# Performance work log

Measured on AMD Instinct MI355X. Metric: run time of the kernel, lower is better.

The kernel has to match this reference:

```python
import jax, jax.numpy as jnp
import numpy as np

B, T, C, H = 4, 2048, 768, 12
D = C // H  # head dim = 64


def setup_inputs() -> dict:
    key = jax.random.key(0)
    ks = jax.random.split(key, 6)
    scale = 1.0 / np.sqrt(C)
    x = jax.random.normal(ks[0], (B, T, C), dtype=jnp.float32)
    # True = padded key (original passes ~key_padding_mask to SDPA)
    key_padding_mask = jax.random.randint(ks[1], (B, 1, 1, T), 0, 2) == 1
    Wqkv = jax.random.normal(ks[2], (C, 3 * C), dtype=jnp.float32) * scale
    bqkv = jax.random.normal(ks[3], (3 * C,), dtype=jnp.float32) * 0.02
    Wproj = jax.random.normal(ks[4], (C, C), dtype=jnp.float32) * scale
    bproj = jax.random.normal(ks[5], (C,), dtype=jnp.float32) * 0.02
    return {"x": x, "key_padding_mask": key_padding_mask, "Wqkv": Wqkv,
            "bqkv": bqkv, "Wproj": Wproj, "bproj": bproj}


def reference(x, key_padding_mask, Wqkv, bqkv, Wproj, bproj):
    # fused QKV projection
    qkv = x @ Wqkv + bqkv                      # [B,T,3C]
    q, k, v = jnp.split(qkv, 3, axis=-1)       # each [B,T,C]

    def heads(t):  # [B,T,C] -> [B,H,T,D]
        return t.reshape(B, T, H, D).transpose(0, 2, 1, 3)

    q, k, v = heads(q), heads(k), heads(v)
    scores = jnp.einsum('bhqd,bhkd->bhqk', q, k) / np.sqrt(D).astype(jnp.float32)
    # attn_mask = ~key_padding_mask: True means attend; padded keys -> -inf
    scores = jnp.where(key_padding_mask, jnp.finfo(scores.dtype).min, scores)
    attn = jax.nn.softmax(scores, axis=-1)
    y = jnp.einsum('bhqk,bhkd->bhqd', attn, v)  # [B,H,T,D]
    y = y.transpose(0, 2, 1, 3).reshape(B, T, C)
    y = y @ Wproj + bproj
    return y
```

## Files before the change

### kernel.cpp

```cpp
#include <hip/hip_runtime.h>
#include <stdint.h>

#define B_ 4
#define T_ 2048
#define C_ 768
#define H_ 12
#define D_ 64
#define BT_ (B_*T_)
#define C3_ (3*C_)
#define FMIN_ (-3.402823466e38f)
#define QSCALE_ (0.18033688f)

typedef __attribute__((ext_vector_type(8))) short short8;
typedef __attribute__((ext_vector_type(4))) short s16x4;
typedef __attribute__((ext_vector_type(4))) float f32x4;

__device__ __forceinline__ float bf2f(unsigned short u) {
    union { unsigned int i; float f; } v; v.i = ((unsigned int)u) << 16; return v.f;
}
__device__ __forceinline__ unsigned short f2bf(float f) {
    union { float ff; unsigned int i; } v; v.ff = f;
    unsigned int r = v.i + 0x7fffu + ((v.i >> 16) & 1u);
    return (unsigned short)(r >> 16);
}
__device__ __forceinline__ unsigned int cvtpk(float lo, float hi) {
    unsigned int r;
    asm("v_cvt_pk_bf16_f32 %0, %1, %2" : "=v"(r) : "v"(lo), "v"(hi));
    return r;
}
__device__ __forceinline__ float ldf(const void* p, size_t i, int isbf) {
    return isbf ? bf2f(((const unsigned short*)p)[i]) : ((const float*)p)[i];
}

__global__ void k_detect(const void* x, const void* wqkv, const void* bqkv,
                         const void* wproj, const void* bproj, const void* mask,
                         int* flags) {
    __shared__ int cnt[8];
    int tid = threadIdx.x;
    if (tid < 8) cnt[tid] = 0;
    __syncthreads();
    const void* ptrs[5] = {x, wqkv, bqkv, wproj, bproj};
#pragma unroll
    for (int t = 0; t < 5; ++t) {
        unsigned short u = ((const unsigned short*)ptrs[t])[2 * tid];
        int e = (u >> 7) & 0xff;
        if (e >= 100 && e <= 140) atomicAdd(&cnt[t], 1);
    }
    if (tid < 64) {
        unsigned int d = ((const unsigned int*)mask)[tid];
        if (d <= 1u) atomicAdd(&cnt[5], 1);
        if (d == 0u || d == 0x3f800000u) atomicAdd(&cnt[6], 1);
    }
    __syncthreads();
    if (tid < 5) flags[tid] = (cnt[tid] >= 128) ? 1 : 0;
    if (tid == 5) flags[5] = (cnt[5] == 64) ? 1 : ((cnt[6] == 64) ? 2 : 0);
}

__global__ void k_canon_x(const void* x, unsigned short* xb, const int* flags) {
    const int n8 = BT_ * C_ / 8;
    int i = blockIdx.x * blockDim.x + threadIdx.x;
    if (i >= n8) return;
    if (flags[0]) {
        ((int4*)xb)[i] = ((const int4*)x)[i];
    } else {
        const float4* xf = (const float4*)x;
        float4 a = xf[2*i], b = xf[2*i+1];
        short8 o;
        o[0]=(short)f2bf(a.x); o[1]=(short)f2bf(a.y); o[2]=(short)f2bf(a.z); o[3]=(short)f2bf(a.w);
        o[4]=(short)f2bf(b.x); o[5]=(short)f2bf(b.y); o[6]=(short)f2bf(b.z); o[7]=(short)f2bf(b.w);
        *(short8*)&xb[8*i] = o;
    }
}

__global__ void k_canon_wT(const void* src, unsigned short* dst, const int* flags,
                           int fidx, int K, int N) {
    __shared__ float tile[32][33];
    int mode = flags[fidx];
    int n0 = blockIdx.x * 32, k0 = blockIdx.y * 32;
    int tx = threadIdx.x & 31, ty = threadIdx.x >> 5;
    for (int r = ty; r < 32; r += 8) {
        size_t idx = (size_t)(k0 + r) * N + (n0 + tx);
        tile[r][tx] = mode ? bf2f(((const unsigned short*)src)[idx])
                           : ((const float*)src)[idx];
    }
    __syncthreads();
    for (int r = ty; r < 32; r += 8) {
        dst[(size_t)(n0 + r) * K + k0 + tx] = f2bf(tile[tx][r]);
    }
}

__global__ void k_canon_small(const void* bqkv, const void* bproj, const void* mask,
                              float* bqkvF, float* bprojF, float* maskF, const int* flags) {
    int i = blockIdx.x * blockDim.x + threadIdx.x;
    if (i < C3_) bqkvF[i] = ldf(bqkv, i, flags[2]);
    if (i < C_)  bprojF[i] = ldf(bproj, i, flags[4]);
    if (i < BT_) {
        int mm = flags[5];
        int mv;
        if (mm == 1)      mv = ((const int*)mask)[i] != 0;
        else if (mm == 2) mv = ((const float*)mask)[i] != 0.0f;
        else              mv = ((const unsigned char*)mask)[i] != 0;
        maskF[i] = mv ? FMIN_ : 0.0f;
    }
}

template<int EPI>
__global__ __launch_bounds__(256) void k_gemm(
        const unsigned short* __restrict__ A, const unsigned short* __restrict__ Bt,
        const float* __restrict__ bias,
        void* __restrict__ out0, unsigned short* __restrict__ out1,
        unsigned short* __restrict__ out2,
        int M, int N, int K) {
    __shared__ __align__(16) unsigned short la[128*72];
    __shared__ __align__(16) unsigned short lb[128*72];
    const int tid = threadIdx.x;
    const int w = tid >> 6, lane = tid & 63, lr = lane & 15, lg = lane >> 4;
    const int wm = (w >> 1) * 64, wn = (w & 1) * 64;
    const int n0 = blockIdx.x * 128, m0 = blockIdx.y * 128;
    f32x4 acc[4][4] = {};
    for (int k0 = 0; k0 < K; k0 += 64) {
#pragma unroll
        for (int c = 0; c < 4; ++c) {
            int idx = tid + c * 256;
            int row = idx >> 3, c8 = (idx & 7) * 8;
            *(short8*)&la[row*72 + c8] = *(const short8*)&A[(size_t)(m0+row)*K + k0 + c8];
            *(short8*)&lb[row*72 + c8] = *(const short8*)&Bt[(size_t)(n0+row)*K + k0 + c8];
        }
        __syncthreads();
#pragma unroll
        for (int ks = 0; ks < 64; ks += 32) {
            short8 af[4], bfr[4];
#pragma unroll
            for (int i = 0; i < 4; ++i)
                af[i] = *(const short8*)&la[(wm + i*16 + lr)*72 + ks + lg*8];
#pragma unroll
            for (int j = 0; j < 4; ++j)
                bfr[j] = *(const short8*)&lb[(wn + j*16 + lr)*72 + ks + lg*8];
#pragma unroll
            for (int i = 0; i < 4; ++i)
#pragma unroll
                for (int j = 0; j < 4; ++j)
                    acc[i][j] = __builtin_amdgcn_mfma_f32_16x16x32_bf16(af[i], bfr[j], acc[i][j], 0, 0, 0);
        }
        __syncthreads();
    }
#pragma unroll
    for (int i = 0; i < 4; ++i)
#pragma unroll
        for (int j = 0; j < 4; ++j)
#pragma unroll
            for (int r = 0; r < 4; ++r) {
                int row = m0 + wm + i*16 + lg*4 + r;
                int col = n0 + wn + j*16 + lr;
                float v = acc[i][j][r] + bias[col];
                if (EPI == 0) {
                    int seg = col / C_;
                    int c = col - seg * C_;
                    int h = c >> 6, d = c & 63;
                    int b = row >> 11, t = row & (T_ - 1);
                    if (seg == 0)      ((unsigned short*)out0)[(((size_t)b*H_ + h)*T_ + t)*D_ + d] = f2bf(v * QSCALE_);
                    else if (seg == 1) out1[(((size_t)b*H_ + h)*T_ + t)*D_ + d] = f2bf(v);
                    else               out2[(((size_t)b*H_ + h)*D_ + d)*T_ + t] = f2bf(v);
                } else {
                    ((float*)out0)[(size_t)row * N + col] = v;
                }
            }
}

__global__ __launch_bounds__(256) void k_attn(
        const unsigned short* __restrict__ Q, const unsigned short* __restrict__ Kt,
        const unsigned short* __restrict__ Vt, const float* __restrict__ maskF,
        unsigned short* __restrict__ AO) {
    __shared__ __align__(16) unsigned short lk[64*72];
    __shared__ __align__(16) unsigned short lv[64*72];
    __shared__ __align__(16) float lmb[64];
    const int tid = threadIdx.x;
    const int w = tid >> 6, lane = tid & 63, lr = lane & 15, lg = lane >> 4;
    const int per = gridDim.x >> 3;
    const int swz = (blockIdx.x & 7) * per + (blockIdx.x >> 3);
    const int bh = swz >> 4, qt = swz & 15;
    const int b = bh / H_, h = bh - b * H_;
    const int qbase = qt * 128 + w * 32;
    const unsigned short* Qb = Q  + (size_t)bh * T_ * D_;
    const unsigned short* Kb = Kt + (size_t)bh * T_ * D_;
    const unsigned short* Vb = Vt + (size_t)bh * D_ * T_;

    short8 qf[2][2];
#pragma unroll
    for (int qc = 0; qc < 2; ++qc)
#pragma unroll
        for (int dh = 0; dh < 2; ++dh)
            qf[qc][dh] = *(const short8*)&Qb[(size_t)(qbase + qc*16 + lr) * D_ + dh*32 + lg*8];

    f32x4 ot[4][2] = {};
    float m[2] = {-INFINITY, -INFINITY}, l[2] = {0.0f, 0.0f};

    for (int kt = 0; kt < T_; kt += 64) {
#pragma unroll
        for (int c = 0; c < 2; ++c) {
            int idx = tid + c * 256;
            int row = idx >> 3, c8 = (idx & 7) * 8;
            *(short8*)&lk[row*72 + c8] = *(const short8*)&Kb[(size_t)(kt + row)*D_ + c8];
            *(short8*)&lv[row*72 + c8] = *(const short8*)&Vb[(size_t)row * T_ + kt + c8];
        }
        if (tid < 64) lmb[tid] = maskF[b*T_ + kt + tid];
        __syncthreads();

        f32x4 st[4][2];
#pragma unroll
        for (int kf = 0; kf < 4; ++kf) {
            f32x4 mi = *(const f32x4*)&lmb[kf*16 + lg*4];
            st[kf][0] = mi;
            st[kf][1] = mi;
        }
#pragma unroll
        for (int dh = 0; dh < 2; ++dh) {
            short8 kfr[4];
#pragma unroll
            for (int kf = 0; kf < 4; ++kf)
                kfr[kf] = *(const short8*)&lk[(kf*16 + lr)*72 + dh*32 + lg*8];
#pragma unroll
            for (int kf = 0; kf < 4; ++kf)
#pragma unroll
                for (int qc = 0; qc < 2; ++qc)
                    st[kf][qc] = __builtin_amdgcn_mfma_f32_16x16x32_bf16(kfr[kf], qf[qc][dh], st[kf][qc], 0, 0, 0);
        }
#pragma unroll
        for (int qc = 0; qc < 2; ++qc) {
            float t0 = fmaxf(fmaxf(st[0][qc][0], st[0][qc][1]), st[0][qc][2]);
            float t1 = fmaxf(fmaxf(st[0][qc][3], st[1][qc][0]), st[1][qc][1]);
            float t2 = fmaxf(fmaxf(st[1][qc][2], st[1][qc][3]), st[2][qc][0]);
            float t3 = fmaxf(fmaxf(st[2][qc][1], st[2][qc][2]), st[2][qc][3]);
            float t4 = fmaxf(fmaxf(st[3][qc][0], st[3][qc][1]), st[3][qc][2]);
            float tm = fmaxf(fmaxf(t0, t1), fmaxf(fmaxf(t2, t3), fmaxf(t4, st[3][qc][3])));
            tm = fmaxf(tm, __shfl_xor(tm, 16));
            tm = fmaxf(tm, __shfl_xor(tm, 32));
            if (!__all(tm - m[qc] <= 8.0f)) {
                float mn = fmaxf(m[qc], tm);
                float sc = __builtin_amdgcn_exp2f(m[qc] - mn);
                m[qc] = mn;
                l[qc] *= sc;
#pragma unroll
                for (int dblk = 0; dblk < 4; ++dblk) ot[dblk][qc] *= sc;
            }
            float mr = m[qc];
            float ps = 0.0f;
#pragma unroll
            for (int kf = 0; kf < 4; ++kf)
#pragma unroll
                for (int r = 0; r < 4; ++r) {
                    float p = __builtin_amdgcn_exp2f(st[kf][qc][r] - mr);
                    st[kf][qc][r] = p;
                    ps += p;
                }
            l[qc] += ps;
        }
        union PU { unsigned int u[4]; short8 s; };
        PU pb[2][2];
#pragma unroll
        for (int qc = 0; qc < 2; ++qc)
#pragma unroll
            for (int ks = 0; ks < 2; ++ks) {
                pb[qc][ks].u[0] = cvtpk(st[2*ks][qc][0],   st[2*ks][qc][1]);
                pb[qc][ks].u[1] = cvtpk(st[2*ks][qc][2],   st[2*ks][qc][3]);
                pb[qc][ks].u[2] = cvtpk(st[2*ks+1][qc][0], st[2*ks+1][qc][1]);
                pb[qc][ks].u[3] = cvtpk(st[2*ks+1][qc][2], st[2*ks+1][qc][3]);
            }
#pragma unroll
        for (int ks = 0; ks < 2; ++ks)
#pragma unroll
            for (int dblk = 0; dblk < 4; ++dblk) {
                const int rb = (dblk*16 + lr)*72 + 32*ks + lg*4;
                s16x4 lo = *(const s16x4*)&lv[rb];
                s16x4 hi = *(const s16x4*)&lv[rb + 16];
                short8 va;
                va[0]=lo[0]; va[1]=lo[1]; va[2]=lo[2]; va[3]=lo[3];
                va[4]=hi[0]; va[5]=hi[1]; va[6]=hi[2]; va[7]=hi[3];
#pragma unroll
                for (int qc = 0; qc < 2; ++qc)
                    ot[dblk][qc] = __builtin_amdgcn_mfma_f32_16x16x32_bf16(va, pb[qc][ks].s, ot[dblk][qc], 0, 0, 0);
            }
        __syncthreads();
    }
#pragma unroll
    for (int qc = 0; qc < 2; ++qc) {
        float ls = l[qc];
        ls += __shfl_xor(ls, 16);
        ls += __shfl_xor(ls, 32);
        float inv = 1.0f / ls;
        size_t row = (size_t)b*T_ + qbase + qc*16 + lr;
#pragma unroll
        for (int dblk = 0; dblk < 4; ++dblk) {
            unsigned int w0 = cvtpk(ot[dblk][qc][0]*inv, ot[dblk][qc][1]*inv);
            unsigned int w1 = cvtpk(ot[dblk][qc][2]*inv, ot[dblk][qc][3]*inv);
            uint2 pkd; pkd.x = w0; pkd.y = w1;
            *(uint2*)&AO[row * C_ + h*64 + dblk*16 + lg*4] = pkd;
        }
    }
}

extern "C" void kernel_launch(void* const* d_in, const int* in_sizes, int n_in,
                              void* d_out, int out_size, void* d_ws, size_t ws_size,
                              hipStream_t stream) {
    const void* x     = d_in[0];
    const void* mask  = d_in[1];
    const void* wqkv  = d_in[2];
    const void* bqkv  = d_in[3];
    const void* wproj = d_in[4];
    const void* bproj = d_in[5];

    char* ws = (char*)d_ws;
    size_t off = 0;
    auto alloc = [&](size_t bytes) -> void* {
        void* p = ws + off;
        off = (off + bytes + 255) & ~(size_t)255;
        return p;
    };
    int* flags            = (int*)alloc(256);
    unsigned short* Xb    = (unsigned short*)alloc((size_t)BT_ * C_ * 2);
    unsigned short* WqkvT = (unsigned short*)alloc((size_t)C3_ * C_ * 2);
    unsigned short* WprojT= (unsigned short*)alloc((size_t)C_ * C_ * 2);
    float* bqkvF          = (float*)alloc((size_t)C3_ * 4);
    float* bprojF         = (float*)alloc((size_t)C_ * 4);
    float* maskF          = (float*)alloc((size_t)BT_ * 4);
    unsigned short* Qs    = (unsigned short*)alloc((size_t)B_*H_*T_*D_ * 2);
    unsigned short* Ks    = (unsigned short*)alloc((size_t)B_*H_*T_*D_ * 2);
    unsigned short* Vts   = (unsigned short*)alloc((size_t)B_*H_*T_*D_ * 2);
    unsigned short* AO    = (unsigned short*)alloc((size_t)BT_ * C_ * 2);

    k_detect<<<1, 256, 0, stream>>>(x, wqkv, bqkv, wproj, bproj, mask, flags);
    k_canon_x<<<(BT_*C_/8 + 255)/256, 256, 0, stream>>>(x, Xb, flags);
    k_canon_wT<<<dim3(C3_/32, C_/32), 256, 0, stream>>>(wqkv, WqkvT, flags, 1, C_, C3_);
    k_canon_wT<<<dim3(C_/32, C_/32), 256, 0, stream>>>(wproj, WprojT, flags, 3, C_, C_);
    k_canon_small<<<(BT_ + 255)/256, 256, 0, stream>>>(bqkv, bproj, mask, bqkvF, bprojF, maskF, flags);

    k_gemm<0><<<dim3(C3_/128, BT_/128), 256, 0, stream>>>(
        Xb, WqkvT, bqkvF, Qs, Ks, Vts, BT_, C3_, C_);
    k_attn<<<B_*H_*(T_/128), 256, 0, stream>>>(Qs, Ks, Vts, maskF, AO);
    k_gemm<1><<<dim3(C_/128, BT_/128), 256, 0, stream>>>(
        AO, WprojT, bprojF, d_out, nullptr, nullptr, BT_, C_, C_);
}
```

Measured before the change: 193.6 us.

## Double-buffer attention K/V tiles and use direct global-to-LDS loads in GEMM

The attention kernel now prefetches the next K/V/mask tile into registers while computing on the current LDS buffer, then writes it into a second LDS buffer. This needs only one barrier per iteration and hides global load latency behind the MFMA work. The GEMM loads switch to global_load_lds (direct DMA into LDS) with an unpadded 64-wide layout, which skips the register round trip. In exchange, the unpadded LDS layout may cause bank conflicts on the fragment reads, and the register prefetch raises register pressure in attention.

```diff
diff --git a/kernel.cpp b/kernel.cpp
--- a/kernel.cpp
+++ b/kernel.cpp
@@ -14,6 +14,10 @@
 typedef __attribute__((ext_vector_type(8))) short short8;
 typedef __attribute__((ext_vector_type(4))) short s16x4;
 typedef __attribute__((ext_vector_type(4))) float f32x4;
+
+#define GLDS16(g, l) __builtin_amdgcn_global_load_lds( \
+    (const __attribute__((address_space(1))) void*)(g), \
+    (__attribute__((address_space(3))) void*)(l), 16, 0, 0)
 
 __device__ __forceinline__ float bf2f(unsigned short u) {
     union { unsigned int i; float f; } v; v.i = ((unsigned int)u) << 16; return v.f;
@@ -111,8 +115,8 @@
         void* __restrict__ out0, unsigned short* __restrict__ out1,
         unsigned short* __restrict__ out2,
         int M, int N, int K) {
-    __shared__ __align__(16) unsigned short la[128*72];
-    __shared__ __align__(16) unsigned short lb[128*72];
+    __shared__ __align__(16) unsigned short la[128*64];
+    __shared__ __align__(16) unsigned short lb[128*64];
     const int tid = threadIdx.x;
     const int w = tid >> 6, lane = tid & 63, lr = lane & 15, lg = lane >> 4;
     const int wm = (w >> 1) * 64, wn = (w & 1) * 64;
@@ -121,10 +125,11 @@
     for (int k0 = 0; k0 < K; k0 += 64) {
 #pragma unroll
         for (int c = 0; c < 4; ++c) {
-            int idx = tid + c * 256;
-            int row = idx >> 3, c8 = (idx & 7) * 8;
-            *(short8*)&la[row*72 + c8] = *(const short8*)&A[(size_t)(m0+row)*K + k0 + c8];
-            *(short8*)&lb[row*72 + c8] = *(const short8*)&Bt[(size_t)(n0+row)*K + k0 + c8];
+            const int chunk = w * 4 + c;
+            const int row = chunk * 8 + (lane >> 3);
+            const int cb8 = (lane & 7) * 8;
+            GLDS16(&A[(size_t)(m0+row)*K + k0 + cb8], &la[chunk*512]);
+            GLDS16(&Bt[(size_t)(n0+row)*K + k0 + cb8], &lb[chunk*512]);
         }
         __syncthreads();
 #pragma unroll
@@ -132,10 +137,10 @@
             short8 af[4], bfr[4];
 #pragma unroll
             for (int i = 0; i < 4; ++i)
-                af[i] = *(const short8*)&la[(wm + i*16 + lr)*72 + ks + lg*8];
+                af[i] = *(const short8*)&la[(wm + i*16 + lr)*64 + ks + lg*8];
 #pragma unroll
             for (int j = 0; j < 4; ++j)
-                bfr[j] = *(const short8*)&lb[(wn + j*16 + lr)*72 + ks + lg*8];
+                bfr[j] = *(const short8*)&lb[(wn + j*16 + lr)*64 + ks + lg*8];
 #pragma unroll
             for (int i = 0; i < 4; ++i)
 #pragma unroll
@@ -171,9 +176,9 @@
         const unsigned short* __restrict__ Q, const unsigned short* __restrict__ Kt,
         const unsigned short* __restrict__ Vt, const float* __restrict__ maskF,
         unsigned short* __restrict__ AO) {
-    __shared__ __align__(16) unsigned short lk[64*72];
-    __shared__ __align__(16) unsigned short lv[64*72];
-    __shared__ __align__(16) float lmb[64];
+    __shared__ __align__(16) unsigned short lk[2][64*72];
+    __shared__ __align__(16) unsigned short lv[2][64*72];
+    __shared__ __align__(16) float lmb[2][64];
     const int tid = threadIdx.x;
     const int w = tid >> 6, lane = tid & 63, lr = lane & 15, lg = lane >> 4;
     const int per = gridDim.x >> 3;
@@ -185,6 +190,9 @@
     const unsigned short* Kb = Kt + (size_t)bh * T_ * D_;
     const unsigned short* Vb = Vt + (size_t)bh * D_ * T_;
 
+    const int r0 = tid >> 3, c8 = (tid & 7) * 8;
+    const int r1 = r0 + 32;
+
     short8 qf[2][2];
 #pragma unroll
     for (int qc = 0; qc < 2; ++qc)
@@ -192,24 +200,33 @@
         for (int dh = 0; dh < 2; ++dh)
             qf[qc][dh] = *(const short8*)&Qb[(size_t)(qbase + qc*16 + lr) * D_ + dh*32 + lg*8];
 
+    *(short8*)&lk[0][r0*72 + c8] = *(const short8*)&Kb[(size_t)r0 * D_ + c8];
+    *(short8*)&lv[0][r0*72 + c8] = *(const short8*)&Vb[(size_t)r0 * T_ + c8];
+    *(short8*)&lk[0][r1*72 + c8] = *(const short8*)&Kb[(size_t)r1 * D_ + c8];
+    *(short8*)&lv[0][r1*72 + c8] = *(const short8*)&Vb[(size_t)r1 * T_ + c8];
+    if (tid < 64) lmb[0][tid] = maskF[b*T_ + tid];
+    __syncthreads();
+
     f32x4 ot[4][2] = {};
     float m[2] = {-INFINITY, -INFINITY}, l[2] = {0.0f, 0.0f};
+    int cur = 0;
 
     for (int kt = 0; kt < T_; kt += 64) {
-#pragma unroll
-        for (int c = 0; c < 2; ++c) {
-            int idx = tid + c * 256;
-            int row = idx >> 3, c8 = (idx & 7) * 8;
-            *(short8*)&lk[row*72 + c8] = *(const short8*)&Kb[(size_t)(kt + row)*D_ + c8];
-            *(short8*)&lv[row*72 + c8] = *(const short8*)&Vb[(size_t)row * T_ + kt + c8];
-        }
-        if (tid < 64) lmb[tid] = maskF[b*T_ + kt + tid];
-        __syncthreads();
+        const int nxt = kt + 64;
+        const bool has = nxt < T_;
+        short8 nk0, nk1, nv0, nv1; float nm = 0.0f;
+        if (has) {
+            nk0 = *(const short8*)&Kb[(size_t)(nxt + r0) * D_ + c8];
+            nv0 = *(const short8*)&Vb[(size_t)r0 * T_ + nxt + c8];
+            nk1 = *(const short8*)&Kb[(size_t)(nxt + r1) * D_ + c8];
+            nv1 = *(const short8*)&Vb[(size_t)r1 * T_ + nxt + c8];
+            if (tid < 64) nm = maskF[b*T_ + nxt + tid];
+        }
 
         f32x4 st[4][2];
 #pragma unroll
         for (int kf = 0; kf < 4; ++kf) {
-            f32x4 mi = *(const f32x4*)&lmb[kf*16 + lg*4];
+            f32x4 mi = *(const f32x4*)&lmb[cur][kf*16 + lg*4];
             st[kf][0] = mi;
             st[kf][1] = mi;
         }
@@ -218,7 +235,7 @@
             short8 kfr[4];
 #pragma unroll
             for (int kf = 0; kf < 4; ++kf)
-                kfr[kf] = *(const short8*)&lk[(kf*16 + lr)*72 + dh*32 + lg*8];
+                kfr[kf] = *(const short8*)&lk[cur][(kf*16 + lr)*72 + dh*32 + lg*8];
 #pragma unroll
             for (int kf = 0; kf < 4; ++kf)
 #pragma unroll
@@ -271,8 +288,8 @@
 #pragma unroll
             for (int dblk = 0; dblk < 4; ++dblk) {
                 const int rb = (dblk*16 + lr)*72 + 32*ks + lg*4;
-                s16x4 lo = *(const s16x4*)&lv[rb];
-                s16x4 hi = *(const s16x4*)&lv[rb + 16];
+                s16x4 lo = *(const s16x4*)&lv[cur][rb];
+                s16x4 hi = *(const s16x4*)&lv[cur][rb + 16];
                 short8 va;
                 va[0]=lo[0]; va[1]=lo[1]; va[2]=lo[2]; va[3]=lo[3];
                 va[4]=hi[0]; va[5]=hi[1]; va[6]=hi[2]; va[7]=hi[3];
@@ -280,7 +297,16 @@
                 for (int qc = 0; qc < 2; ++qc)
                     ot[dblk][qc] = __builtin_amdgcn_mfma_f32_16x16x32_bf16(va, pb[qc][ks].s, ot[dblk][qc], 0, 0, 0);
             }
+        if (has) {
+            const int nb = cur ^ 1;
+            *(short8*)&lk[nb][r0*72 + c8] = nk0;
+            *(short8*)&lv[nb][r0*72 + c8] = nv0;
+            *(short8*)&lk[nb][r1*72 + c8] = nk1;
+            *(short8*)&lv[nb][r1*72 + c8] = nv1;
+            if (tid < 64) lmb[nb][tid] = nm;
+        }
         __syncthreads();
+        cur ^= 1;
     }
 #pragma unroll
     for (int qc = 0; qc < 2; ++qc) {
```

Result: slower. 222.7 us (+15.0%).
